# Performance work log

Measured on AMD Instinct MI355X. Metric: run time of the kernel, lower is better.

Reference implementation:

```python
import jax, jax.numpy as jnp
import numpy as np

B, T, C = 2, 2048, 1024
NH = 16
HD = C // NH
SCALE = 1.0 / np.sqrt(HD).astype(np.float32)


def setup_inputs() -> dict:
    key = jax.random.key(0)
    k1, k2, k3 = jax.random.split(key, 3)
    x = jax.random.normal(k1, (B, T, C), dtype=jnp.float32)
    # torch Linear stores weight (out,in) and computes x @ W^T; we store the
    # transposed (in,out) layout directly, scaled like default init.
    w_qkv = jax.random.normal(k2, (C, 3 * C), dtype=jnp.float32) * (1.0 / np.sqrt(C))
    w_proj = jax.random.normal(k3, (C, C), dtype=jnp.float32) * (1.0 / np.sqrt(C))
    return {"x": x, "w_qkv": w_qkv, "w_proj": w_proj}


def reference(x, w_qkv, w_proj):
    b, t, c = x.shape
    qkv = x @ w_qkv                                  # (b, t, 3c)
    q, k, v = jnp.split(qkv, 3, axis=-1)
    q = q.reshape(b, t, NH, HD)
    k = k.reshape(b, t, NH, HD)
    v = v.reshape(b, t, NH, HD)
    # scores: (b, nh, t, t) — full materialization, faithful to the original
    att = jnp.einsum("bthd,bshd->bhts", q, k) * SCALE
    causal = jnp.tril(jnp.ones((t, t), dtype=bool))  # (t, t)
    neg = jnp.finfo(att.dtype).min
    att = jnp.where(causal[None, None, :, :], att, neg)
    weights = jax.nn.softmax(att, axis=-1)
    y = jnp.einsum("bhts,bshd->bthd", weights, v).reshape(b, t, c)
    y = y @ w_proj
    return y
```

## Files before the change

### kernel.cpp

```cpp
#include <hip/hip_runtime.h>
#include <hip/hip_bf16.h>
#include <stdint.h>

typedef __bf16 bf16x8 __attribute__((ext_vector_type(8)));
typedef float f32x4 __attribute__((ext_vector_type(4)));
typedef unsigned short us4v __attribute__((ext_vector_type(4)));
typedef unsigned short us8v __attribute__((ext_vector_type(8)));

#define B_   2
#define T_   2048
#define C_   1024
#define NH_  16
#define HD_  64

__device__ __forceinline__ unsigned short f2bf(float f) {
  unsigned int u = __builtin_bit_cast(unsigned int, f);
  u += 0x7fffu + ((u >> 16) & 1u);
  return (unsigned short)(u >> 16);
}
__device__ __forceinline__ float bf2f(unsigned short u) {
  unsigned int x = ((unsigned int)u) << 16;
  return __builtin_bit_cast(float, x);
}

__device__ __forceinline__ void gload16(const void* g, void* l) {
  __builtin_amdgcn_global_load_lds(
      (const __attribute__((address_space(1))) unsigned int*)g,
      (__attribute__((address_space(3))) unsigned int*)l, 16, 0, 0);
}

__device__ __forceinline__ f32x4 mfma16(bf16x8 a, bf16x8 b, f32x4 c) {
  return __builtin_amdgcn_mfma_f32_16x16x32_bf16(a, b, c, 0, 0, 0);
}

__global__ __launch_bounds__(256) void cast_x_kernel(const float4* __restrict__ in,
                                                     us4v* __restrict__ out) {
  int i = blockIdx.x * 256 + threadIdx.x;
  float4 f = in[i];
  us4v o; o[0] = f2bf(f.x); o[1] = f2bf(f.y); o[2] = f2bf(f.z); o[3] = f2bf(f.w);
  out[i] = o;
}

__global__ __launch_bounds__(256) void transpose_cast_kernel(const float* __restrict__ w,
                                                             unsigned short* __restrict__ wT,
                                                             int K, int N) {
  __shared__ float tile[32][33];
  int n0 = blockIdx.x * 32, k0 = blockIdx.y * 32;
  int tx = threadIdx.x, ty = threadIdx.y;
  #pragma unroll
  for (int i = 0; i < 4; ++i)
    tile[ty + 8*i][tx] = w[(size_t)(k0 + ty + 8*i) * N + n0 + tx];
  __syncthreads();
  #pragma unroll
  for (int i = 0; i < 4; ++i)
    wT[(size_t)(n0 + ty + 8*i) * K + k0 + tx] = f2bf(tile[tx][ty + 8*i]);
}

__device__ __forceinline__ void gemm_core(const unsigned short* __restrict__ A,
                                          const unsigned short* __restrict__ Bt,
                                          int K, int m0, int n0,
                                          unsigned short* lA, unsigned short* lB,
                                          f32x4 acc[4][4]) {
  const int t = threadIdx.x;
  const int lane = t & 63, w = t >> 6;
  const int wm = w >> 1, wn = w & 1;
  const int g = lane >> 4, r16 = lane & 15;
  #pragma unroll
  for (int i = 0; i < 4; ++i)
    #pragma unroll
    for (int j = 0; j < 4; ++j) acc[i][j] = (f32x4){0.f, 0.f, 0.f, 0.f};

  for (int k0 = 0; k0 < K; k0 += 64) {
    #pragma unroll
    for (int i = 0; i < 4; ++i) {
      int slot = i * 256 + t;
      int r = slot >> 3, p = slot & 7;
      int q = p ^ (r & 7);
      gload16(A  + (size_t)(m0 + r) * K + k0 + q * 8, lA + slot * 8);
      gload16(Bt + (size_t)(n0 + r) * K + k0 + q * 8, lB + slot * 8);
    }
    asm volatile("s_waitcnt vmcnt(0)" ::: "memory");
    __syncthreads();

    bf16x8 af[4][2], bfr[4][2];
    #pragma unroll
    for (int mi = 0; mi < 4; ++mi)
      #pragma unroll
      for (int kk = 0; kk < 2; ++kk) {
        int r = wm * 64 + mi * 16 + r16;
        int ps = (kk * 4 + g) ^ (r & 7);
        af[mi][kk] = *(const bf16x8*)(lA + r * 64 + ps * 8);
      }
    #pragma unroll
    for (int ni = 0; ni < 4; ++ni)
      #pragma unroll
      for (int kk = 0; kk < 2; ++kk) {
        int r = wn * 64 + ni * 16 + r16;
        int ps = (kk * 4 + g) ^ (r & 7);
        bfr[ni][kk] = *(const bf16x8*)(lB + r * 64 + ps * 8);
      }
    #pragma unroll
    for (int mi = 0; mi < 4; ++mi)
      #pragma unroll
      for (int ni = 0; ni < 4; ++ni)
        #pragma unroll
        for (int kk = 0; kk < 2; ++kk)
          acc[mi][ni] = mfma16(af[mi][kk], bfr[ni][kk], acc[mi][ni]);
    __syncthreads();
  }
}

__device__ __forceinline__ int xcd_swz(int flat, int nwg) {
  int cpx = nwg >> 3;
  return (flat & 7) * cpx + (flat >> 3);
}

__global__ __launch_bounds__(256) void gemm_qkv_kernel(const unsigned short* __restrict__ xb,
                                                       const unsigned short* __restrict__ wT,
                                                       unsigned short* __restrict__ qb,
                                                       unsigned short* __restrict__ kb,
                                                       unsigned short* __restrict__ vb) {
  __shared__ unsigned short lA[128 * 64];
  __shared__ unsigned short lB[128 * 64];
  f32x4 acc[4][4];
  const int nbx = 3 * C_ / 128;
  int flat = xcd_swz(blockIdx.y * nbx + blockIdx.x, nbx * ((B_ * T_) / 128));
  const int m0 = (flat / nbx) * 128, n0 = (flat % nbx) * 128;
  gemm_core(xb, wT, C_, m0, n0, lA, lB, acc);
  const int t = threadIdx.x, lane = t & 63, w = t >> 6;
  const int wm = w >> 1, wn = w & 1, g = lane >> 4, r16 = lane & 15;
  #pragma unroll
  for (int mi = 0; mi < 4; ++mi)
    #pragma unroll
    for (int ni = 0; ni < 4; ++ni)
      #pragma unroll
      for (int j = 0; j < 4; ++j) {
        int gm = m0 + wm * 64 + mi * 16 + g * 4 + j;
        int gn = n0 + wn * 64 + ni * 16 + r16;
        int b = gm >> 11, tt = gm & 2047;
        int s = gn >> 10, rem = gn & 1023;
        int h = rem >> 6, d = rem & 63;
        unsigned short val = f2bf(acc[mi][ni][j]);
        size_t idx = ((size_t)(b * NH_ + h) * T_ + tt) * HD_ + d;
        if (s == 0)      qb[idx] = val;
        else if (s == 1) kb[idx] = val;
        else             vb[idx] = val;
      }
}

__global__ __launch_bounds__(256) void gemm_proj_kernel(const unsigned short* __restrict__ ab,
                                                        const unsigned short* __restrict__ wT,
                                                        float* __restrict__ out) {
  __shared__ unsigned short lA[128 * 64];
  __shared__ unsigned short lB[128 * 64];
  f32x4 acc[4][4];
  const int nbx = C_ / 128;
  int flat = xcd_swz(blockIdx.y * nbx + blockIdx.x, nbx * ((B_ * T_) / 128));
  const int m0 = (flat / nbx) * 128, n0 = (flat % nbx) * 128;
  gemm_core(ab, wT, C_, m0, n0, lA, lB, acc);
  const int t = threadIdx.x, lane = t & 63, w = t >> 6;
  const int wm = w >> 1, wn = w & 1, g = lane >> 4, r16 = lane & 15;
  #pragma unroll
  for (int mi = 0; mi < 4; ++mi)
    #pragma unroll
    for (int ni = 0; ni < 4; ++ni)
      #pragma unroll
      for (int j = 0; j < 4; ++j) {
        int gm = m0 + wm * 64 + mi * 16 + g * 4 + j;
        int gn = n0 + wn * 64 + ni * 16 + r16;
        out[(size_t)gm * C_ + gn] = acc[mi][ni][j];
      }
}

__global__ __launch_bounds__(256, 3) void attn_kernel(const unsigned short* __restrict__ qb,
                                                      const unsigned short* __restrict__ kb,
                                                      const unsigned short* __restrict__ vb,
                                                      unsigned short* __restrict__ ao) {
  __shared__ unsigned short LDS[16384];
  const int pairIdx = blockIdx.x, bh = blockIdx.y;
  const int t = threadIdx.x, lane = t & 63, w4 = t >> 6;
  const int g = lane >> 4, r16 = lane & 15;
  const int sel = w4 >> 1, halfsel = w4 & 1;
  const int tileBase = sel ? (31 - pairIdx) : pairIdx;
  const int qt0 = tileBase * 64 + halfsel * 32;
  const int myNt = tileBase + 1;
  const int ntMax = 32 - pairIdx;

  const unsigned short* Q  = qb + (size_t)bh * (T_ * HD_);
  const unsigned short* Kp = kb + (size_t)bh * (T_ * HD_);
  const unsigned short* Vp = vb + (size_t)bh * (T_ * HD_);

  bf16x8 qf[2][2];
  #pragma unroll
  for (int h = 0; h < 2; ++h) {
    int qrow = qt0 + h * 16 + r16;
    #pragma unroll
    for (int kk = 0; kk < 2; ++kk) {
      us8v raw = *(const us8v*)(Q + (size_t)qrow * HD_ + kk * 32 + g * 8);
      bf16x8 qv;
      #pragma unroll
      for (int j = 0; j < 8; ++j) qv[j] = (__bf16)(bf2f(raw[j]) * 0.125f);
      qf[h][kk] = qv;
    }
  }

  f32x4 o[2][4];
  #pragma unroll
  for (int h = 0; h < 2; ++h)
    #pragma unroll
    for (int c = 0; c < 4; ++c) o[h][c] = (f32x4){0.f, 0.f, 0.f, 0.f};
  float mrun[2] = {-__builtin_inff(), -__builtin_inff()};
  float lrun[2] = {0.f, 0.f};

  const int kr0 = t >> 3,        kp0 = (t & 7) ^ (kr0 & 7);
  const int kr1 = (t + 256) >> 3, kp1 = (t & 7) ^ (kr1 & 7);
  const int colp = (lane & 32) | ((lane & 12) << 1) | ((lane >> 2) & 4) | (lane & 3);
  const int cslot = colp >> 3, cwithin = colp & 7;

  gload16(Kp + (size_t)kr0 * HD_ + kp0 * 8, LDS + t * 8);
  gload16(Kp + (size_t)kr1 * HD_ + kp1 * 8, LDS + (t + 256) * 8);
  us8v nv0 = *(const us8v*)(Vp + (size_t)lane * HD_ + w4 * 16);
  us8v nv1 = *(const us8v*)(Vp + (size_t)lane * HD_ + w4 * 16 + 8);

  for (int it = 0; it < ntMax; ++it) {
    const int cur = it & 1;
    const unsigned short* Kl = LDS + cur * 4096;
    unsigned short* Vt = LDS + 8192 + cur * 4096;

    asm volatile("s_waitcnt vmcnt(0)" ::: "memory");
    #pragma unroll
    for (int u = 0; u < 8; ++u) {
      int d = w4 * 16 + u;
      Vt[d * 64 + ((cslot ^ u) << 3) + cwithin] = nv0[u];
    }
    #pragma unroll
    for (int u = 0; u < 8; ++u) {
      int d = w4 * 16 + 8 + u;
      Vt[d * 64 + ((cslot ^ u) << 3) + cwithin] = nv1[u];
    }
    __syncthreads();

    if (it + 1 < ntMax) {
      const int kv0n = (it + 1) * 64;
      unsigned short* Kn = LDS + (cur ^ 1) * 4096;
      gload16(Kp + (size_t)(kv0n + kr0) * HD_ + kp0 * 8, Kn + t * 8);
      gload16(Kp + (size_t)(kv0n + kr1) * HD_ + kp1 * 8, Kn + (t + 256) * 8);
      nv0 = *(const us8v*)(Vp + (size_t)(kv0n + lane) * HD_ + w4 * 16);
      nv1 = *(const us8v*)(Vp + (size_t)(kv0n + lane) * HD_ + w4 * 16 + 8);
    }

    if (it < myNt) {
      f32x4 s4t[2][4];
      #pragma unroll
      for (int h = 0; h < 2; ++h)
        #pragma unroll
        for (int c = 0; c < 4; ++c) s4t[h][c] = (f32x4){0.f, 0.f, 0.f, 0.f};
      #pragma unroll
      for (int c = 0; c < 4; ++c)
        #pragma unroll
        for (int kk = 0; kk < 2; ++kk) {
          int r = c * 16 + r16;
          int ps = (kk * 4 + g) ^ (r & 7);
          bf16x8 kf = *(const bf16x8*)(Kl + r * 64 + ps * 8);
          s4t[0][c] = mfma16(kf, qf[0][kk], s4t[0][c]);
          s4t[1][c] = mfma16(kf, qf[1][kk], s4t[1][c]);
        }
      if (it == myNt - 1) {
        #pragma unroll
        for (int h = 0; h < 2; ++h) {
          int qloc = halfsel * 32 + h * 16 + r16;
          #pragma unroll
          for (int c = 0; c < 4; ++c)
            #pragma unroll
            for (int j = 0; j < 4; ++j)
              if (c * 16 + g * 4 + j > qloc) s4t[h][c][j] = -1e30f;
        }
      }
      bf16x8 pf[2][2];
      #pragma unroll
      for (int h = 0; h < 2; ++h) {
        float mx = -1e30f;
        #pragma unroll
        for (int c = 0; c < 4; ++c)
          #pragma unroll
          for (int j = 0; j < 4; ++j) mx = fmaxf(mx, s4t[h][c][j]);
        mx = fmaxf(mx, __shfl_xor(mx, 16));
        mx = fmaxf(mx, __shfl_xor(mx, 32));
        float mn = fmaxf(mrun[h], mx);
        float alpha = __expf(mrun[h] - mn);
        mrun[h] = mn;
        float rs = 0.f;
        #pragma unroll
        for (int c = 0; c < 4; ++c)
          #pragma unroll
          for (int j = 0; j < 4; ++j) {
            float p = __expf(s4t[h][c][j] - mn);
            s4t[h][c][j] = p;
            rs += p;
          }
        rs += __shfl_xor(rs, 16);
        rs += __shfl_xor(rs, 32);
        lrun[h] = lrun[h] * alpha + rs;
        #pragma unroll
        for (int c = 0; c < 4; ++c)
          #pragma unroll
          for (int j = 0; j < 4; ++j) o[h][c][j] *= alpha;
        #pragma unroll
        for (int kk = 0; kk < 2; ++kk) {
          bf16x8 p;
          #pragma unroll
          for (int j = 0; j < 4; ++j) {
            p[j]     = (__bf16)s4t[h][2 * kk][j];
            p[4 + j] = (__bf16)s4t[h][2 * kk + 1][j];
          }
          pf[h][kk] = p;
        }
      }
      #pragma unroll
      for (int c = 0; c < 4; ++c) {
        int rv = c * 16 + r16;
        #pragma unroll
        for (int kk = 0; kk < 2; ++kk) {
          int slot = (4 * kk + g) ^ (r16 & 7);
          bf16x8 vf = *(const bf16x8*)(Vt + rv * 64 + slot * 8);
          o[0][c] = mfma16(vf, pf[0][kk], o[0][c]);
          o[1][c] = mfma16(vf, pf[1][kk], o[1][c]);
        }
      }
    }
  }

  const int deadK = ((ntMax - 1) & 1) ^ 1;
  unsigned short* ep = LDS + deadK * 4096 + w4 * 1024;
  #pragma unroll
  for (int h = 0; h < 2; ++h) {
    float inv = 1.f / lrun[h];
    #pragma unroll
    for (int c = 0; c < 4; ++c) {
      us4v pk;
      #pragma unroll
      for (int j = 0; j < 4; ++j) pk[j] = f2bf(o[h][c][j] * inv);
      int slot = (4 * c + g) ^ r16;
      *(us4v*)(ep + r16 * 64 + slot * 4) = pk;
    }
    asm volatile("s_waitcnt lgkmcnt(0)" ::: "memory");
    __builtin_amdgcn_sched_barrier(0);
    {
      int q = lane >> 2, seg = lane & 3;
      us4v a0 = *(const us4v*)(ep + q * 64 + (((seg * 4 + 0) ^ q) & 15) * 4);
      us4v a1 = *(const us4v*)(ep + q * 64 + (((seg * 4 + 1) ^ q) & 15) * 4);
      us4v a2 = *(const us4v*)(ep + q * 64 + (((seg * 4 + 2) ^ q) & 15) * 4);
      us4v a3 = *(const us4v*)(ep + q * 64 + (((seg * 4 + 3) ^ q) & 15) * 4);
      us8v o0 = {a0[0],a0[1],a0[2],a0[3],a1[0],a1[1],a1[2],a1[3]};
      us8v o1 = {a2[0],a2[1],a2[2],a2[3],a3[0],a3[1],a3[2],a3[3]};
      size_t rowg = (size_t)(bh >> 4) * T_ + qt0 + h * 16 + q;
      int colg = (bh & 15) * 64 + seg * 16;
      *(us8v*)(ao + rowg * C_ + colg)     = o0;
      *(us8v*)(ao + rowg * C_ + colg + 8) = o1;
    }
    asm volatile("s_waitcnt lgkmcnt(0)" ::: "memory");
    __builtin_amdgcn_sched_barrier(0);
  }
}

extern "C" void kernel_launch(void* const* d_in, const int* in_sizes, int n_in,
                              void* d_out, int out_size, void* d_ws, size_t ws_size,
                              hipStream_t stream) {
  const float* x      = (const float*)d_in[0];
  const float* w_qkv  = (const float*)d_in[1];
  const float* w_proj = (const float*)d_in[2];
  float* out = (float*)d_out;
  char* ws = (char*)d_ws;

  unsigned short* xb     = (unsigned short*)(ws);
  unsigned short* wqkvT  = (unsigned short*)(ws + 8388608);
  unsigned short* wprojT = (unsigned short*)(ws + 14680064);
  unsigned short* qb     = (unsigned short*)(ws + 16777216);
  unsigned short* kb     = (unsigned short*)(ws + 25165824);
  unsigned short* vb     = (unsigned short*)(ws + 33554432);
  unsigned short* ao     = xb;

  cast_x_kernel<<<4096, 256, 0, stream>>>((const float4*)x, (us4v*)xb);
  transpose_cast_kernel<<<dim3(3 * C_ / 32, C_ / 32), dim3(32, 8), 0, stream>>>(
      w_qkv, wqkvT, C_, 3 * C_);
  transpose_cast_kernel<<<dim3(C_ / 32, C_ / 32), dim3(32, 8), 0, stream>>>(
      w_proj, wprojT, C_, C_);
  gemm_qkv_kernel<<<dim3(3 * C_ / 128, (B_ * T_) / 128), 256, 0, stream>>>(
      xb, wqkvT, qb, kb, vb);
  attn_kernel<<<dim3(16, 32), 256, 0, stream>>>(qb, kb, vb, ao);
  gemm_proj_kernel<<<dim3(C_ / 128, (B_ * T_) / 128), 256, 0, stream>>>(
      ao, wprojT, out);
}
```

Baseline: 126.7 us.

## Replace paired causal-tile attention blocks with one 128-thread block per query tile

```diff
diff --git a/kernel.cpp b/kernel.cpp
--- a/kernel.cpp
+++ b/kernel.cpp
@@ -172,19 +172,16 @@
       }
 }
 
-__global__ __launch_bounds__(256, 3) void attn_kernel(const unsigned short* __restrict__ qb,
+__global__ __launch_bounds__(128, 2) void attn_kernel(const unsigned short* __restrict__ qb,
                                                       const unsigned short* __restrict__ kb,
                                                       const unsigned short* __restrict__ vb,
                                                       unsigned short* __restrict__ ao) {
   __shared__ unsigned short LDS[16384];
-  const int pairIdx = blockIdx.x, bh = blockIdx.y;
+  const int tile = 31 - blockIdx.x, bh = blockIdx.y;
   const int t = threadIdx.x, lane = t & 63, w4 = t >> 6;
   const int g = lane >> 4, r16 = lane & 15;
-  const int sel = w4 >> 1, halfsel = w4 & 1;
-  const int tileBase = sel ? (31 - pairIdx) : pairIdx;
-  const int qt0 = tileBase * 64 + halfsel * 32;
-  const int myNt = tileBase + 1;
-  const int ntMax = 32 - pairIdx;
+  const int qt0 = tile * 64 + w4 * 32;
+  const int nt = tile + 1;
 
   const unsigned short* Q  = qb + (size_t)bh * (T_ * HD_);
   const unsigned short* Kp = kb + (size_t)bh * (T_ * HD_);
@@ -212,17 +209,24 @@
   float mrun[2] = {-__builtin_inff(), -__builtin_inff()};
   float lrun[2] = {0.f, 0.f};
 
-  const int kr0 = t >> 3,        kp0 = (t & 7) ^ (kr0 & 7);
-  const int kr1 = (t + 256) >> 3, kp1 = (t & 7) ^ (kr1 & 7);
+  const int kr0 = (t +   0) >> 3, kp0 = (t & 7) ^ (kr0 & 7);
+  const int kr1 = (t + 128) >> 3, kp1 = (t & 7) ^ (kr1 & 7);
+  const int kr2 = (t + 256) >> 3, kp2 = (t & 7) ^ (kr2 & 7);
+  const int kr3 = (t + 384) >> 3, kp3 = (t & 7) ^ (kr3 & 7);
   const int colp = (lane & 32) | ((lane & 12) << 1) | ((lane >> 2) & 4) | (lane & 3);
   const int cslot = colp >> 3, cwithin = colp & 7;
-
-  gload16(Kp + (size_t)kr0 * HD_ + kp0 * 8, LDS + t * 8);
-  gload16(Kp + (size_t)kr1 * HD_ + kp1 * 8, LDS + (t + 256) * 8);
-  us8v nv0 = *(const us8v*)(Vp + (size_t)lane * HD_ + w4 * 16);
-  us8v nv1 = *(const us8v*)(Vp + (size_t)lane * HD_ + w4 * 16 + 8);
-
-  for (int it = 0; it < ntMax; ++it) {
+  const int voct = 4 * w4;
+
+  gload16(Kp + (size_t)kr0 * HD_ + kp0 * 8, LDS + (t +   0) * 8);
+  gload16(Kp + (size_t)kr1 * HD_ + kp1 * 8, LDS + (t + 128) * 8);
+  gload16(Kp + (size_t)kr2 * HD_ + kp2 * 8, LDS + (t + 256) * 8);
+  gload16(Kp + (size_t)kr3 * HD_ + kp3 * 8, LDS + (t + 384) * 8);
+  us8v nv0 = *(const us8v*)(Vp + (size_t)lane * HD_ + (voct + 0) * 8);
+  us8v nv1 = *(const us8v*)(Vp + (size_t)lane * HD_ + (voct + 1) * 8);
+  us8v nv2 = *(const us8v*)(Vp + (size_t)lane * HD_ + (voct + 2) * 8);
+  us8v nv3 = *(const us8v*)(Vp + (size_t)lane * HD_ + (voct + 3) * 8);
+
+  for (int it = 0; it < nt; ++it) {
     const int cur = it & 1;
     const unsigned short* Kl = LDS + cur * 4096;
     unsigned short* Vt = LDS + 8192 + cur * 4096;
@@ -230,26 +234,40 @@
     asm volatile("s_waitcnt vmcnt(0)" ::: "memory");
     #pragma unroll
     for (int u = 0; u < 8; ++u) {
-      int d = w4 * 16 + u;
+      int d = (voct + 0) * 8 + u;
       Vt[d * 64 + ((cslot ^ u) << 3) + cwithin] = nv0[u];
     }
     #pragma unroll
     for (int u = 0; u < 8; ++u) {
-      int d = w4 * 16 + 8 + u;
+      int d = (voct + 1) * 8 + u;
       Vt[d * 64 + ((cslot ^ u) << 3) + cwithin] = nv1[u];
     }
+    #pragma unroll
+    for (int u = 0; u < 8; ++u) {
+      int d = (voct + 2) * 8 + u;
+      Vt[d * 64 + ((cslot ^ u) << 3) + cwithin] = nv2[u];
+    }
+    #pragma unroll
+    for (int u = 0; u < 8; ++u) {
+      int d = (voct + 3) * 8 + u;
+      Vt[d * 64 + ((cslot ^ u) << 3) + cwithin] = nv3[u];
+    }
     __syncthreads();
 
-    if (it + 1 < ntMax) {
+    if (it + 1 < nt) {
       const int kv0n = (it + 1) * 64;
       unsigned short* Kn = LDS + (cur ^ 1) * 4096;
-      gload16(Kp + (size_t)(kv0n + kr0) * HD_ + kp0 * 8, Kn + t * 8);
-      gload16(Kp + (size_t)(kv0n + kr1) * HD_ + kp1 * 8, Kn + (t + 256) * 8);
-      nv0 = *(const us8v*)(Vp + (size_t)(kv0n + lane) * HD_ + w4 * 16);
-      nv1 = *(const us8v*)(Vp + (size_t)(kv0n + lane) * HD_ + w4 * 16 + 8);
-    }
-
-    if (it < myNt) {
+      gload16(Kp + (size_t)(kv0n + kr0) * HD_ + kp0 * 8, Kn + (t +   0) * 8);
+      gload16(Kp + (size_t)(kv0n + kr1) * HD_ + kp1 * 8, Kn + (t + 128) * 8);
+      gload16(Kp + (size_t)(kv0n + kr2) * HD_ + kp2 * 8, Kn + (t + 256) * 8);
+      gload16(Kp + (size_t)(kv0n + kr3) * HD_ + kp3 * 8, Kn + (t + 384) * 8);
+      nv0 = *(const us8v*)(Vp + (size_t)(kv0n + lane) * HD_ + (voct + 0) * 8);
+      nv1 = *(const us8v*)(Vp + (size_t)(kv0n + lane) * HD_ + (voct + 1) * 8);
+      nv2 = *(const us8v*)(Vp + (size_t)(kv0n + lane) * HD_ + (voct + 2) * 8);
+      nv3 = *(const us8v*)(Vp + (size_t)(kv0n + lane) * HD_ + (voct + 3) * 8);
+    }
+
+    {
       f32x4 s4t[2][4];
       #pragma unroll
       for (int h = 0; h < 2; ++h)
@@ -265,10 +283,10 @@
           s4t[0][c] = mfma16(kf, qf[0][kk], s4t[0][c]);
           s4t[1][c] = mfma16(kf, qf[1][kk], s4t[1][c]);
         }
-      if (it == myNt - 1) {
+      if (it == nt - 1) {
         #pragma unroll
         for (int h = 0; h < 2; ++h) {
-          int qloc = halfsel * 32 + h * 16 + r16;
+          int qloc = w4 * 32 + h * 16 + r16;
           #pragma unroll
           for (int c = 0; c < 4; ++c)
             #pragma unroll
@@ -330,7 +348,7 @@
     }
   }
 
-  const int deadK = ((ntMax - 1) & 1) ^ 1;
+  const int deadK = ((nt - 1) & 1) ^ 1;
   unsigned short* ep = LDS + deadK * 4096 + w4 * 1024;
   #pragma unroll
   for (int h = 0; h < 2; ++h) {
@@ -387,7 +405,7 @@
       w_proj, wprojT, C_, C_);
   gemm_qkv_kernel<<<dim3(3 * C_ / 128, (B_ * T_) / 128), 256, 0, stream>>>(
       xb, wqkvT, qb, kb, vb);
-  attn_kernel<<<dim3(16, 32), 256, 0, stream>>>(qb, kb, vb, ao);
+  attn_kernel<<<dim3(32, 32), 128, 0, stream>>>(qb, kb, vb, ao);
   gemm_proj_kernel<<<dim3(C_ / 128, (B_ * T_) / 128), 256, 0, stream>>>(
       ao, wprojT, out);
 }
```

New measurement: 137.4 us. 1.08x slower.

## Process two 64-key tiles per pipeline epoch in attention kernel

Applied to the files above, without the earlier changes.

```diff
diff --git a/kernel.cpp b/kernel.cpp
--- a/kernel.cpp
+++ b/kernel.cpp
@@ -172,19 +172,20 @@
       }
 }
 
-__global__ __launch_bounds__(256, 3) void attn_kernel(const unsigned short* __restrict__ qb,
+__global__ __launch_bounds__(256, 2) void attn_kernel(const unsigned short* __restrict__ qb,
                                                       const unsigned short* __restrict__ kb,
                                                       const unsigned short* __restrict__ vb,
                                                       unsigned short* __restrict__ ao) {
-  __shared__ unsigned short LDS[16384];
+  __shared__ unsigned short LDS[32768];
   const int pairIdx = blockIdx.x, bh = blockIdx.y;
   const int t = threadIdx.x, lane = t & 63, w4 = t >> 6;
   const int g = lane >> 4, r16 = lane & 15;
   const int sel = w4 >> 1, halfsel = w4 & 1;
-  const int tileBase = sel ? (31 - pairIdx) : pairIdx;
-  const int qt0 = tileBase * 64 + halfsel * 32;
-  const int myNt = tileBase + 1;
+  const int tile = sel ? (31 - pairIdx) : pairIdx;
+  const int qt0 = tile * 64 + halfsel * 32;
+  const int myNt = tile + 1;
   const int ntMax = 32 - pairIdx;
+  const int epochs = (ntMax + 1) >> 1;
 
   const unsigned short* Q  = qb + (size_t)bh * (T_ * HD_);
   const unsigned short* Kp = kb + (size_t)bh * (T_ * HD_);
@@ -212,49 +213,68 @@
   float mrun[2] = {-__builtin_inff(), -__builtin_inff()};
   float lrun[2] = {0.f, 0.f};
 
-  const int kr0 = t >> 3,        kp0 = (t & 7) ^ (kr0 & 7);
+  const int kr0 = (t +   0) >> 3, kp0 = (t & 7) ^ (kr0 & 7);
   const int kr1 = (t + 256) >> 3, kp1 = (t & 7) ^ (kr1 & 7);
+  const int kr2 = (t + 512) >> 3, kp2 = (t & 7) ^ (kr2 & 7);
+  const int kr3 = (t + 768) >> 3, kp3 = (t & 7) ^ (kr3 & 7);
   const int colp = (lane & 32) | ((lane & 12) << 1) | ((lane >> 2) & 4) | (lane & 3);
   const int cslot = colp >> 3, cwithin = colp & 7;
-
-  gload16(Kp + (size_t)kr0 * HD_ + kp0 * 8, LDS + t * 8);
+  const int oct0 = 2 * w4, oct1 = 2 * w4 + 1;
+
+  gload16(Kp + (size_t)kr0 * HD_ + kp0 * 8, LDS + (t +   0) * 8);
   gload16(Kp + (size_t)kr1 * HD_ + kp1 * 8, LDS + (t + 256) * 8);
-  us8v nv0 = *(const us8v*)(Vp + (size_t)lane * HD_ + w4 * 16);
-  us8v nv1 = *(const us8v*)(Vp + (size_t)lane * HD_ + w4 * 16 + 8);
-
-  for (int it = 0; it < ntMax; ++it) {
-    const int cur = it & 1;
-    const unsigned short* Kl = LDS + cur * 4096;
-    unsigned short* Vt = LDS + 8192 + cur * 4096;
+  gload16(Kp + (size_t)kr2 * HD_ + kp2 * 8, LDS + (t + 512) * 8);
+  gload16(Kp + (size_t)kr3 * HD_ + kp3 * 8, LDS + (t + 768) * 8);
+  us8v nv00 = *(const us8v*)(Vp + (size_t)lane * HD_ + oct0 * 8);
+  us8v nv01 = *(const us8v*)(Vp + (size_t)lane * HD_ + oct1 * 8);
+  us8v nv10 = *(const us8v*)(Vp + (size_t)(lane + 64) * HD_ + oct0 * 8);
+  us8v nv11 = *(const us8v*)(Vp + (size_t)(lane + 64) * HD_ + oct1 * 8);
+
+  for (int e = 0; e < epochs; ++e) {
+    const int cur = e & 1;
+    const unsigned short* Kl = LDS + cur * 8192;
+    unsigned short* Vt = LDS + 16384 + cur * 8192;
 
     asm volatile("s_waitcnt vmcnt(0)" ::: "memory");
     #pragma unroll
     for (int u = 0; u < 8; ++u) {
-      int d = w4 * 16 + u;
-      Vt[d * 64 + ((cslot ^ u) << 3) + cwithin] = nv0[u];
+      int d = oct0 * 8 + u;
+      Vt[d * 128 + ((cslot ^ u) << 3) + cwithin] = nv00[u];
     }
     #pragma unroll
     for (int u = 0; u < 8; ++u) {
-      int d = w4 * 16 + 8 + u;
-      Vt[d * 64 + ((cslot ^ u) << 3) + cwithin] = nv1[u];
+      int d = oct1 * 8 + u;
+      Vt[d * 128 + ((cslot ^ u) << 3) + cwithin] = nv01[u];
+    }
+    #pragma unroll
+    for (int u = 0; u < 8; ++u) {
+      int d = oct0 * 8 + u;
+      Vt[d * 128 + 64 + ((cslot ^ u) << 3) + cwithin] = nv10[u];
+    }
+    #pragma unroll
+    for (int u = 0; u < 8; ++u) {
+      int d = oct1 * 8 + u;
+      Vt[d * 128 + 64 + ((cslot ^ u) << 3) + cwithin] = nv11[u];
     }
     __syncthreads();
 
-    if (it + 1 < ntMax) {
-      const int kv0n = (it + 1) * 64;
-      unsigned short* Kn = LDS + (cur ^ 1) * 4096;
-      gload16(Kp + (size_t)(kv0n + kr0) * HD_ + kp0 * 8, Kn + t * 8);
-      gload16(Kp + (size_t)(kv0n + kr1) * HD_ + kp1 * 8, Kn + (t + 256) * 8);
-      nv0 = *(const us8v*)(Vp + (size_t)(kv0n + lane) * HD_ + w4 * 16);
-      nv1 = *(const us8v*)(Vp + (size_t)(kv0n + lane) * HD_ + w4 * 16 + 8);
-    }
-
-    if (it < myNt) {
-      f32x4 s4t[2][4];
-      #pragma unroll
-      for (int h = 0; h < 2; ++h)
-        #pragma unroll
-        for (int c = 0; c < 4; ++c) s4t[h][c] = (f32x4){0.f, 0.f, 0.f, 0.f};
+    if (e + 1 < epochs) {
+      const int kw = (e + 1) * 128;
+      unsigned short* Kn = LDS + (cur ^ 1) * 8192;
+      gload16(Kp + (size_t)(kw + kr0) * HD_ + kp0 * 8, Kn + (t +   0) * 8);
+      gload16(Kp + (size_t)(kw + kr1) * HD_ + kp1 * 8, Kn + (t + 256) * 8);
+      gload16(Kp + (size_t)(kw + kr2) * HD_ + kp2 * 8, Kn + (t + 512) * 8);
+      gload16(Kp + (size_t)(kw + kr3) * HD_ + kp3 * 8, Kn + (t + 768) * 8);
+      nv00 = *(const us8v*)(Vp + (size_t)(kw + lane) * HD_ + oct0 * 8);
+      nv01 = *(const us8v*)(Vp + (size_t)(kw + lane) * HD_ + oct1 * 8);
+      nv10 = *(const us8v*)(Vp + (size_t)(kw + lane + 64) * HD_ + oct0 * 8);
+      nv11 = *(const us8v*)(Vp + (size_t)(kw + lane + 64) * HD_ + oct1 * 8);
+    }
+
+    const int t0 = 2 * e, t1 = 2 * e + 1;
+    const bool act0 = t0 < myNt, act1 = t1 < myNt;
+    if (act0) {
+      f32x4 s4t[2][8];
       #pragma unroll
       for (int c = 0; c < 4; ++c)
         #pragma unroll
@@ -262,10 +282,33 @@
           int r = c * 16 + r16;
           int ps = (kk * 4 + g) ^ (r & 7);
           bf16x8 kf = *(const bf16x8*)(Kl + r * 64 + ps * 8);
-          s4t[0][c] = mfma16(kf, qf[0][kk], s4t[0][c]);
-          s4t[1][c] = mfma16(kf, qf[1][kk], s4t[1][c]);
+          if (kk == 0) { s4t[0][c] = mfma16(kf, qf[0][0], (f32x4){0,0,0,0});
+                         s4t[1][c] = mfma16(kf, qf[1][0], (f32x4){0,0,0,0}); }
+          else         { s4t[0][c] = mfma16(kf, qf[0][1], s4t[0][c]);
+                         s4t[1][c] = mfma16(kf, qf[1][1], s4t[1][c]); }
         }
-      if (it == myNt - 1) {
+      if (act1) {
+        #pragma unroll
+        for (int c = 0; c < 4; ++c)
+          #pragma unroll
+          for (int kk = 0; kk < 2; ++kk) {
+            int r = 64 + c * 16 + r16;
+            int ps = (kk * 4 + g) ^ (r & 7);
+            bf16x8 kf = *(const bf16x8*)(Kl + r * 64 + ps * 8);
+            if (kk == 0) { s4t[0][4 + c] = mfma16(kf, qf[0][0], (f32x4){0,0,0,0});
+                           s4t[1][4 + c] = mfma16(kf, qf[1][0], (f32x4){0,0,0,0}); }
+            else         { s4t[0][4 + c] = mfma16(kf, qf[0][1], s4t[0][4 + c]);
+                           s4t[1][4 + c] = mfma16(kf, qf[1][1], s4t[1][4 + c]); }
+          }
+      } else {
+        #pragma unroll
+        for (int h = 0; h < 2; ++h)
+          #pragma unroll
+          for (int c = 0; c < 4; ++c)
+            s4t[h][4 + c] = (f32x4){-1e30f, -1e30f, -1e30f, -1e30f};
+      }
+      if (t0 == myNt - 1 || (act1 && t1 == myNt - 1)) {
+        const int dsub = (t0 == myNt - 1) ? 0 : 4;
         #pragma unroll
         for (int h = 0; h < 2; ++h) {
           int qloc = halfsel * 32 + h * 16 + r16;
@@ -273,15 +316,15 @@
           for (int c = 0; c < 4; ++c)
             #pragma unroll
             for (int j = 0; j < 4; ++j)
-              if (c * 16 + g * 4 + j > qloc) s4t[h][c][j] = -1e30f;
+              if (c * 16 + g * 4 + j > qloc) s4t[h][dsub + c][j] = -1e30f;
         }
       }
-      bf16x8 pf[2][2];
+      bf16x8 pf[2][2][2];
       #pragma unroll
       for (int h = 0; h < 2; ++h) {
         float mx = -1e30f;
         #pragma unroll
-        for (int c = 0; c < 4; ++c)
+        for (int c = 0; c < 8; ++c)
           #pragma unroll
           for (int j = 0; j < 4; ++j) mx = fmaxf(mx, s4t[h][c][j]);
         mx = fmaxf(mx, __shfl_xor(mx, 16));
@@ -291,7 +334,7 @@
         mrun[h] = mn;
         float rs = 0.f;
         #pragma unroll
-        for (int c = 0; c < 4; ++c)
+        for (int c = 0; c < 8; ++c)
           #pragma unroll
           for (int j = 0; j < 4; ++j) {
             float p = __expf(s4t[h][c][j] - mn);
@@ -306,15 +349,17 @@
           #pragma unroll
           for (int j = 0; j < 4; ++j) o[h][c][j] *= alpha;
         #pragma unroll
-        for (int kk = 0; kk < 2; ++kk) {
-          bf16x8 p;
-          #pragma unroll
-          for (int j = 0; j < 4; ++j) {
-            p[j]     = (__bf16)s4t[h][2 * kk][j];
-            p[4 + j] = (__bf16)s4t[h][2 * kk + 1][j];
+        for (int s = 0; s < 2; ++s)
+          #pragma unroll
+          for (int kk = 0; kk < 2; ++kk) {
+            bf16x8 p;
+            #pragma unroll
+            for (int j = 0; j < 4; ++j) {
+              p[j]     = (__bf16)s4t[h][s * 4 + 2 * kk][j];
+              p[4 + j] = (__bf16)s4t[h][s * 4 + 2 * kk + 1][j];
+            }
+            pf[h][s][kk] = p;
           }
-          pf[h][kk] = p;
-        }
       }
       #pragma unroll
       for (int c = 0; c < 4; ++c) {
@@ -322,16 +367,29 @@
         #pragma unroll
         for (int kk = 0; kk < 2; ++kk) {
           int slot = (4 * kk + g) ^ (r16 & 7);
-          bf16x8 vf = *(const bf16x8*)(Vt + rv * 64 + slot * 8);
-          o[0][c] = mfma16(vf, pf[0][kk], o[0][c]);
-          o[1][c] = mfma16(vf, pf[1][kk], o[1][c]);
+          bf16x8 vf = *(const bf16x8*)(Vt + rv * 128 + slot * 8);
+          o[0][c] = mfma16(vf, pf[0][0][kk], o[0][c]);
+          o[1][c] = mfma16(vf, pf[1][0][kk], o[1][c]);
         }
       }
+      if (act1) {
+        #pragma unroll
+        for (int c = 0; c < 4; ++c) {
+          int rv = c * 16 + r16;
+          #pragma unroll
+          for (int kk = 0; kk < 2; ++kk) {
+            int slot = (4 * kk + g) ^ (r16 & 7);
+            bf16x8 vf = *(const bf16x8*)(Vt + rv * 128 + 64 + slot * 8);
+            o[0][c] = mfma16(vf, pf[0][1][kk], o[0][c]);
+            o[1][c] = mfma16(vf, pf[1][1][kk], o[1][c]);
+          }
+        }
+      }
     }
   }
 
-  const int deadK = ((ntMax - 1) & 1) ^ 1;
-  unsigned short* ep = LDS + deadK * 4096 + w4 * 1024;
+  const int deadK = ((epochs - 1) & 1) ^ 1;
+  unsigned short* ep = LDS + deadK * 8192 + w4 * 1024;
   #pragma unroll
   for (int h = 0; h < 2; ++h) {
     float inv = 1.f / lrun[h];
```

After: 207.9 us. 1.64x slower.
